# Optimization experiments

Hardware: AMD Instinct MI355X
Metric: run time of the kernel (lower is better)

Reference implementation:

```python
import jax, jax.numpy as jnp
import numpy as np

B, S, L, F = 32, 512, 13, 768
H = 512


def setup_inputs() -> dict:
    key = jax.random.key(0)
    ks = jax.random.split(key, 9)
    x = jax.random.normal(ks[0], (B, S, L, F), dtype=jnp.float32)
    lengths = jax.random.randint(ks[1], (B,), 0, S)
    lw = jnp.ones((L,), dtype=jnp.float32)  # WeightedAverage weights
    s1 = 1.0 / np.sqrt(2 * F)
    s2 = 1.0 / np.sqrt(H)
    s3 = 1.0 / np.sqrt(H // 2)
    W1 = jax.random.uniform(ks[2], (2 * F, H), jnp.float32, -s1, s1)
    b1 = jax.random.uniform(ks[3], (H,), jnp.float32, -s1, s1)
    W2 = jax.random.uniform(ks[4], (H, H // 2), jnp.float32, -s2, s2)
    b2 = jax.random.uniform(ks[5], (H // 2,), jnp.float32, -s2, s2)
    W3 = jax.random.uniform(ks[6], (H // 2, 1), jnp.float32, -s3, s3)
    b3 = jax.random.uniform(ks[7], (1,), jnp.float32, -s3, s3)
    return {"x": x, "lengths": lengths, "lw": lw, "W1": W1, "b1": b1,
            "W2": W2, "b2": b2, "W3": W3, "b3": b3}


def reference(x, lengths, lw, W1, b1, W2, b2, W3, b3):
    # layer-weighted average: softmax over L, contract layer dim
    w = jax.nn.softmax(lw)
    word = jnp.einsum("bslf,l->bsf", x, w)  # [B,S,F]

    # masked mean/std over the first lengths[i] positions of each sequence
    seq_len = word.shape[1]
    mask = (jnp.arange(seq_len)[None, :] < lengths[:, None]).astype(word.dtype)  # [B,S]
    n = jnp.sum(mask, axis=1, keepdims=True)  # [B,1]
    mean = jnp.sum(word * mask[:, :, None], axis=1) / jnp.maximum(n, 1.0)  # [B,F]
    diff = (word - mean[:, None, :]) * mask[:, :, None]
    # torch.std is unbiased (ddof=1); std defined 0 when n<=1
    var = jnp.sum(diff * diff, axis=1) / jnp.maximum(n - 1.0, 1.0)
    std = jnp.where(n > 1.0, jnp.sqrt(var), 0.0)
    feats = jnp.concatenate([mean, std], axis=-1)  # [B,2F]

    # MLP (dropout is inference no-op)
    h = jax.nn.relu(feats @ W1 + b1)
    h = jax.nn.relu(h @ W2 + b2)
    return h @ W3 + b3  # [B,1]
```

## Files before the change

kernel.cpp:

```cpp
#include <hip/hip_runtime.h>
#include <hip/hip_bf16.h>

#define LNUM 13
#define FDIM 768
#define SDIM 512
#define BNUM 32
#define H1DIM 512
#define H2DIM 256
#define GA0 992
#define GPAD (GA0 + BNUM)


__global__ __launch_bounds__(192) void kA_partials(
    const float* __restrict__ x, const int* __restrict__ lengths,
    const float* __restrict__ lw, float* __restrict__ partial) {
  __shared__ int lenS[BNUM];
  __shared__ int BB[BNUM + 1];
  __shared__ float wS[LNUM];
  const int tid = threadIdx.x;

  if (tid < BNUM) lenS[tid] = lengths[tid];
  __syncthreads();
  if (tid == 0) {
    int T = 0;
    #pragma unroll
    for (int b = 0; b < BNUM; ++b) T += lenS[b];
    int acc = 0; BB[0] = 0;
    #pragma unroll
    for (int b = 0; b < BNUM; ++b) {
      int nb = (T > 0 && lenS[b] > 0) ? (lenS[b] * GA0 + T - 1) / T : 0;
      acc += nb; BB[b + 1] = acc;
    }
    float m = lw[0];
    #pragma unroll
    for (int l = 1; l < LNUM; ++l) m = fmaxf(m, lw[l]);
    float e[LNUM]; float s = 0.f;
    #pragma unroll
    for (int l = 0; l < LNUM; ++l) { e[l] = expf(lw[l] - m); s += e[l]; }
    #pragma unroll
    for (int l = 0; l < LNUM; ++l) wS[l] = e[l] / s;
  }
  __syncthreads();

  const int g = blockIdx.x;
  if (g >= BB[BNUM]) return;

  int lo = 0, hi = BNUM;
  while (hi - lo > 1) { int mid = (lo + hi) >> 1; if (g >= BB[mid]) lo = mid; else hi = mid; }
  const int b   = lo;
  const int i   = g - BB[b];
  const int n   = BB[b + 1] - BB[b];
  const int len = lenS[b];
  const int base = len / n, rem = len % n;
  const int s0 = i * base + min(i, rem);
  const int cnt = base + (i < rem ? 1 : 0);

  float4 sum = make_float4(0.f, 0.f, 0.f, 0.f);
  float4 sq  = make_float4(0.f, 0.f, 0.f, 0.f);
  const float* xb = x + (size_t)b * SDIM * (LNUM * FDIM) + (size_t)tid * 4;

  for (int s = s0; s < s0 + cnt; ++s) {
    const float* xs = xb + (size_t)s * (LNUM * FDIM);
    float4 word = make_float4(0.f, 0.f, 0.f, 0.f);
    #pragma unroll
    for (int l = 0; l < LNUM; ++l) {
      float4 v = *reinterpret_cast<const float4*>(xs + l * FDIM);
      const float wl = wS[l];
      word.x = fmaf(wl, v.x, word.x);
      word.y = fmaf(wl, v.y, word.y);
      word.z = fmaf(wl, v.z, word.z);
      word.w = fmaf(wl, v.w, word.w);
    }
    sum.x += word.x; sum.y += word.y; sum.z += word.z; sum.w += word.w;
    sq.x = fmaf(word.x, word.x, sq.x);
    sq.y = fmaf(word.y, word.y, sq.y);
    sq.z = fmaf(word.z, word.z, sq.z);
    sq.w = fmaf(word.w, word.w, sq.w);
  }

  float* p = partial + (size_t)g * (2 * FDIM) + (size_t)tid * 4;
  *reinterpret_cast<float4*>(p) = sum;
  *reinterpret_cast<float4*>(p + FDIM) = sq;
}

__global__ __launch_bounds__(256) void kStats(
    const float* __restrict__ partial, const int* __restrict__ lengths,
    float* __restrict__ feats) {
  const int b  = blockIdx.x / 12;
  const int cg = blockIdx.x % 12;
  const int cl = threadIdx.x & 63;
  const int k  = threadIdx.x >> 6;
  const int f  = cg * 64 + cl;

  __shared__ int lenS[BNUM];
  __shared__ int BB[BNUM + 1];
  if (threadIdx.x < BNUM) lenS[threadIdx.x] = lengths[threadIdx.x];
  __syncthreads();
  if (threadIdx.x == 0) {
    int T = 0;
    #pragma unroll
    for (int bb = 0; bb < BNUM; ++bb) T += lenS[bb];
    int acc = 0; BB[0] = 0;
    #pragma unroll
    for (int bb = 0; bb < BNUM; ++bb) {
      int nb = (T > 0 && lenS[bb] > 0) ? (lenS[bb] * GA0 + T - 1) / T : 0;
      acc += nb; BB[bb + 1] = acc;
    }
  }
  __syncthreads();

  const int cBeg = BB[b], cEnd = BB[b + 1];
  float ms = 0.f, mq = 0.f;
  for (int cc = cBeg + k; cc < cEnd; cc += 4) {
    const float* p = partial + (size_t)cc * (2 * FDIM);
    ms += p[f];
    mq += p[FDIM + f];
  }
  __shared__ float rs[4][64], rq[4][64];
  rs[k][cl] = ms; rq[k][cl] = mq;
  __syncthreads();

  if (threadIdx.x < 64) {
    ms = rs[0][cl] + rs[1][cl] + rs[2][cl] + rs[3][cl];
    mq = rq[0][cl] + rq[1][cl] + rq[2][cl] + rq[3][cl];
    const int n = lenS[b];
    const float fn = (float)n;
    const float mean = ms / fmaxf(fn, 1.f);
    const float var = (mq - fn * mean * mean) / fmaxf(fn - 1.f, 1.f);
    const float sd = (n > 1) ? sqrtf(fmaxf(var, 0.f)) : 0.f;
    feats[(size_t)b * 2 * FDIM + f] = mean;
    feats[(size_t)b * 2 * FDIM + FDIM + f] = sd;
  }
}

__global__ __launch_bounds__(512) void kFC1(
    const float* __restrict__ feats, const float* __restrict__ W1,
    const float* __restrict__ b1, float* __restrict__ h1) {
  const int b  = blockIdx.x >> 2;
  const int jt = blockIdx.x & 3;
  const int t  = threadIdx.x;
  const int jl = t & 127;
  const int kh = t >> 7;
  const int j  = jt * 128 + jl;

  __shared__ float fs[2 * FDIM];
  __shared__ float red[4][128];

  for (int i = t; i < 2 * FDIM; i += 512)
    fs[i] = feats[(size_t)b * 2 * FDIM + i];
  __syncthreads();

  const float* wcol = W1 + (size_t)kh * 384 * H1DIM + j;
  const float* fk = fs + kh * 384;
  float acc = 0.f;
  #pragma unroll 16
  for (int i = 0; i < 384; ++i)
    acc = fmaf(fk[i], wcol[(size_t)i * H1DIM], acc);
  red[kh][jl] = acc;
  __syncthreads();

  if (t < 128) {
    float a = red[0][t] + red[1][t] + red[2][t] + red[3][t] + b1[jt * 128 + t];
    h1[(size_t)b * H1DIM + jt * 128 + t] = fmaxf(a, 0.f);
  }
}

__global__ __launch_bounds__(512) void kFC23(
    const float* __restrict__ h1, const float* __restrict__ W2,
    const float* __restrict__ b2, const float* __restrict__ W3,
    const float* __restrict__ b3, float* __restrict__ out) {
  const int b = blockIdx.x;
  const int t = threadIdx.x;
  const int jl = t & 255;
  const int kh = t >> 8;

  __shared__ float hs[H1DIM];
  __shared__ float red[2 * H2DIM];
  __shared__ float wred[8];

  if (t < H1DIM) hs[t] = h1[(size_t)b * H1DIM + t];
  __syncthreads();

  const float* wcol = W2 + (size_t)kh * 256 * H2DIM + jl;
  const float* hk = hs + kh * 256;
  float acc = 0.f;
  #pragma unroll 16
  for (int i = 0; i < 256; ++i)
    acc = fmaf(hk[i], wcol[(size_t)i * H2DIM], acc);
  red[kh * H2DIM + jl] = acc;
  __syncthreads();

  float v = 0.f;
  if (t < H2DIM) {
    const float h2 = fmaxf(red[t] + red[H2DIM + t] + b2[t], 0.f);
    v = h2 * W3[t];
  }
  #pragma unroll
  for (int off = 32; off > 0; off >>= 1) v += __shfl_down(v, off, 64);
  if ((t & 63) == 0) wred[t >> 6] = v;
  __syncthreads();
  if (t == 0) {
    float r = b3[0];
    #pragma unroll
    for (int i = 0; i < 8; ++i) r += wred[i];
    out[b] = r;
  }
}

extern "C" void kernel_launch(void* const* d_in, const int* in_sizes, int n_in,
                              void* d_out, int out_size, void* d_ws, size_t ws_size,
                              hipStream_t stream) {
  const float* x       = (const float*)d_in[0];
  const int*   lengths = (const int*)  d_in[1];
  const float* lw      = (const float*)d_in[2];
  const float* W1      = (const float*)d_in[3];
  const float* b1      = (const float*)d_in[4];
  const float* W2      = (const float*)d_in[5];
  const float* b2      = (const float*)d_in[6];
  const float* W3      = (const float*)d_in[7];
  const float* b3      = (const float*)d_in[8];
  float* out = (float*)d_out;

  float* partial = (float*)d_ws;
  float* feats   = partial + (size_t)GPAD * 2 * FDIM;
  float* h1      = feats + (size_t)BNUM * 2 * FDIM;

  kA_partials<<<dim3(GPAD), dim3(192), 0, stream>>>(x, lengths, lw, partial);
  kStats<<<dim3(BNUM * 12), dim3(256), 0, stream>>>(partial, lengths, feats);
  kFC1<<<dim3(BNUM * 4), dim3(512), 0, stream>>>(feats, W1, b1, h1);
  kFC23<<<dim3(BNUM), dim3(512), 0, stream>>>(h1, W2, b2, W3, b3, out);
}
```

Before: 89.27 us.

## Fuse FC1 and FC2/FC3 into one MLP kernel and raise partial-block count

Merges the two MLP kernels into a single per-batch kernel. FC1 now uses float4 weight loads per thread across all 512 outputs, and h1 stays in shared memory, which removes one launch and a global round trip. Separately, the number of sequence-chunk blocks in the partials kernel goes from 992 to 1504 to improve occupancy on the bandwidth-bound reduction. The fused MLP runs only 32 blocks, so FC1 parallelism drops from 128 blocks to 32.

```diff
diff --git a/kernel.cpp b/kernel.cpp
--- a/kernel.cpp
+++ b/kernel.cpp
@@ -7,7 +7,7 @@
 #define BNUM 32
 #define H1DIM 512
 #define H2DIM 256
-#define GA0 992
+#define GA0 1504
 #define GPAD (GA0 + BNUM)
 
 
@@ -133,61 +133,61 @@
   }
 }
 
-__global__ __launch_bounds__(512) void kFC1(
-    const float* __restrict__ feats, const float* __restrict__ W1,
-    const float* __restrict__ b1, float* __restrict__ h1) {
-  const int b  = blockIdx.x >> 2;
-  const int jt = blockIdx.x & 3;
-  const int t  = threadIdx.x;
-  const int jl = t & 127;
-  const int kh = t >> 7;
-  const int j  = jt * 128 + jl;
+__global__ __launch_bounds__(512) void kMLP(
+    const float* __restrict__ feats,
+    const float* __restrict__ W1, const float* __restrict__ b1,
+    const float* __restrict__ W2, const float* __restrict__ b2,
+    const float* __restrict__ W3, const float* __restrict__ b3,
+    float* __restrict__ out) {
+  const int b = blockIdx.x;
+  const int t = threadIdx.x;
 
   __shared__ float fs[2 * FDIM];
-  __shared__ float red[4][128];
+  __shared__ float r1[4][H1DIM];
+  __shared__ float h1s[H1DIM];
+  __shared__ float red[2 * H2DIM];
+  __shared__ float wred[8];
 
   for (int i = t; i < 2 * FDIM; i += 512)
     fs[i] = feats[(size_t)b * 2 * FDIM + i];
   __syncthreads();
 
-  const float* wcol = W1 + (size_t)kh * 384 * H1DIM + j;
-  const float* fk = fs + kh * 384;
-  float acc = 0.f;
-  #pragma unroll 16
-  for (int i = 0; i < 384; ++i)
-    acc = fmaf(fk[i], wcol[(size_t)i * H1DIM], acc);
-  red[kh][jl] = acc;
-  __syncthreads();
-
-  if (t < 128) {
-    float a = red[0][t] + red[1][t] + red[2][t] + red[3][t] + b1[jt * 128 + t];
-    h1[(size_t)b * H1DIM + jt * 128 + t] = fmaxf(a, 0.f);
-  }
-}
-
-__global__ __launch_bounds__(512) void kFC23(
-    const float* __restrict__ h1, const float* __restrict__ W2,
-    const float* __restrict__ b2, const float* __restrict__ W3,
-    const float* __restrict__ b3, float* __restrict__ out) {
-  const int b = blockIdx.x;
-  const int t = threadIdx.x;
-  const int jl = t & 255;
-  const int kh = t >> 8;
-
-  __shared__ float hs[H1DIM];
-  __shared__ float red[2 * H2DIM];
-  __shared__ float wred[8];
-
-  if (t < H1DIM) hs[t] = h1[(size_t)b * H1DIM + t];
-  __syncthreads();
-
-  const float* wcol = W2 + (size_t)kh * 256 * H2DIM + jl;
-  const float* hk = hs + kh * 256;
-  float acc = 0.f;
-  #pragma unroll 16
-  for (int i = 0; i < 256; ++i)
-    acc = fmaf(hk[i], wcol[(size_t)i * H2DIM], acc);
-  red[kh * H2DIM + jl] = acc;
+  {
+    const int jq = t & 127;
+    const int kh = t >> 7;
+    const float* fk = fs + kh * 384;
+    const float* wrow = W1 + (size_t)kh * 384 * H1DIM + 4 * jq;
+    float4 acc = make_float4(0.f, 0.f, 0.f, 0.f);
+    #pragma unroll 8
+    for (int i = 0; i < 384; ++i) {
+      float4 wv = *reinterpret_cast<const float4*>(wrow + (size_t)i * H1DIM);
+      const float f = fk[i];
+      acc.x = fmaf(f, wv.x, acc.x);
+      acc.y = fmaf(f, wv.y, acc.y);
+      acc.z = fmaf(f, wv.z, acc.z);
+      acc.w = fmaf(f, wv.w, acc.w);
+    }
+    r1[kh][4 * jq]     = acc.x;
+    r1[kh][4 * jq + 1] = acc.y;
+    r1[kh][4 * jq + 2] = acc.z;
+    r1[kh][4 * jq + 3] = acc.w;
+  }
+  __syncthreads();
+  if (t < H1DIM)
+    h1s[t] = fmaxf(r1[0][t] + r1[1][t] + r1[2][t] + r1[3][t] + b1[t], 0.f);
+  __syncthreads();
+
+  {
+    const int jl = t & 255;
+    const int kh = t >> 8;
+    const float* wcol = W2 + (size_t)kh * 256 * H2DIM + jl;
+    const float* hk = h1s + kh * 256;
+    float acc = 0.f;
+    #pragma unroll 16
+    for (int i = 0; i < 256; ++i)
+      acc = fmaf(hk[i], wcol[(size_t)i * H2DIM], acc);
+    red[kh * H2DIM + jl] = acc;
+  }
   __syncthreads();
 
   float v = 0.f;
@@ -223,10 +223,8 @@
 
   float* partial = (float*)d_ws;
   float* feats   = partial + (size_t)GPAD * 2 * FDIM;
-  float* h1      = feats + (size_t)BNUM * 2 * FDIM;
 
   kA_partials<<<dim3(GPAD), dim3(192), 0, stream>>>(x, lengths, lw, partial);
   kStats<<<dim3(BNUM * 12), dim3(256), 0, stream>>>(partial, lengths, feats);
-  kFC1<<<dim3(BNUM * 4), dim3(512), 0, stream>>>(feats, W1, b1, h1);
-  kFC23<<<dim3(BNUM), dim3(512), 0, stream>>>(h1, W2, b2, W3, b3, out);
-}
+  kMLP<<<dim3(BNUM), dim3(512), 0, stream>>>(feats, W1, b1, W2, b2, W3, b3, out);
+}
```

Result: slower. 112.7 us (+26.2%).

## Fuse partial-sum and stats kernels with a device-wide atomic counter barrier

Applied to the files above, without the earlier changes.

Merges the x-reduction kernel and the per-feature statistics kernel into one launch. Every block bumps an atomic counter after writing its partials, and the first 384 blocks spin until all blocks are done before reducing partials into mean and std. The goal is to drop one kernel launch boundary. In exchange it adds a memset launch and spin-wait latency, and it depends on all blocks being co-resident or scheduled before the waiters starve them.

```diff
diff --git a/kernel.cpp b/kernel.cpp
--- a/kernel.cpp
+++ b/kernel.cpp
@@ -9,15 +9,18 @@
 #define H2DIM 256
 #define GA0 992
 #define GPAD (GA0 + BNUM)
-
-
-__global__ __launch_bounds__(192) void kA_partials(
+#define NSTATS (BNUM * 12)
+
+__global__ __launch_bounds__(192) void kAS(
     const float* __restrict__ x, const int* __restrict__ lengths,
-    const float* __restrict__ lw, float* __restrict__ partial) {
+    const float* __restrict__ lw, float* __restrict__ partial,
+    float* __restrict__ feats, unsigned int* __restrict__ done) {
   __shared__ int lenS[BNUM];
   __shared__ int BB[BNUM + 1];
   __shared__ float wS[LNUM];
+  __shared__ float rs[3][64], rq[3][64];
   const int tid = threadIdx.x;
+  const int g = blockIdx.x;
 
   if (tid < BNUM) lenS[tid] = lengths[tid];
   __syncthreads();
@@ -42,87 +45,77 @@
   }
   __syncthreads();
 
-  const int g = blockIdx.x;
-  if (g >= BB[BNUM]) return;
-
-  int lo = 0, hi = BNUM;
-  while (hi - lo > 1) { int mid = (lo + hi) >> 1; if (g >= BB[mid]) lo = mid; else hi = mid; }
-  const int b   = lo;
-  const int i   = g - BB[b];
-  const int n   = BB[b + 1] - BB[b];
-  const int len = lenS[b];
-  const int base = len / n, rem = len % n;
-  const int s0 = i * base + min(i, rem);
-  const int cnt = base + (i < rem ? 1 : 0);
-
-  float4 sum = make_float4(0.f, 0.f, 0.f, 0.f);
-  float4 sq  = make_float4(0.f, 0.f, 0.f, 0.f);
-  const float* xb = x + (size_t)b * SDIM * (LNUM * FDIM) + (size_t)tid * 4;
-
-  for (int s = s0; s < s0 + cnt; ++s) {
-    const float* xs = xb + (size_t)s * (LNUM * FDIM);
-    float4 word = make_float4(0.f, 0.f, 0.f, 0.f);
-    #pragma unroll
-    for (int l = 0; l < LNUM; ++l) {
-      float4 v = *reinterpret_cast<const float4*>(xs + l * FDIM);
-      const float wl = wS[l];
-      word.x = fmaf(wl, v.x, word.x);
-      word.y = fmaf(wl, v.y, word.y);
-      word.z = fmaf(wl, v.z, word.z);
-      word.w = fmaf(wl, v.w, word.w);
+  if (g < BB[BNUM]) {
+    int lo = 0, hi = BNUM;
+    while (hi - lo > 1) { int mid = (lo + hi) >> 1; if (g >= BB[mid]) lo = mid; else hi = mid; }
+    const int b   = lo;
+    const int i   = g - BB[b];
+    const int n   = BB[b + 1] - BB[b];
+    const int len = lenS[b];
+    const int base = len / n, rem = len % n;
+    const int s0 = i * base + min(i, rem);
+    const int cnt = base + (i < rem ? 1 : 0);
+
+    float4 sum = make_float4(0.f, 0.f, 0.f, 0.f);
+    float4 sq  = make_float4(0.f, 0.f, 0.f, 0.f);
+    const float* xb = x + (size_t)b * SDIM * (LNUM * FDIM) + (size_t)tid * 4;
+
+    for (int s = s0; s < s0 + cnt; ++s) {
+      const float* xs = xb + (size_t)s * (LNUM * FDIM);
+      float4 word = make_float4(0.f, 0.f, 0.f, 0.f);
+      #pragma unroll
+      for (int l = 0; l < LNUM; ++l) {
+        float4 v = *reinterpret_cast<const float4*>(xs + l * FDIM);
+        const float wl = wS[l];
+        word.x = fmaf(wl, v.x, word.x);
+        word.y = fmaf(wl, v.y, word.y);
+        word.z = fmaf(wl, v.z, word.z);
+        word.w = fmaf(wl, v.w, word.w);
+      }
+      sum.x += word.x; sum.y += word.y; sum.z += word.z; sum.w += word.w;
+      sq.x = fmaf(word.x, word.x, sq.x);
+      sq.y = fmaf(word.y, word.y, sq.y);
+      sq.z = fmaf(word.z, word.z, sq.z);
+      sq.w = fmaf(word.w, word.w, sq.w);
     }
-    sum.x += word.x; sum.y += word.y; sum.z += word.z; sum.w += word.w;
-    sq.x = fmaf(word.x, word.x, sq.x);
-    sq.y = fmaf(word.y, word.y, sq.y);
-    sq.z = fmaf(word.z, word.z, sq.z);
-    sq.w = fmaf(word.w, word.w, sq.w);
-  }
-
-  float* p = partial + (size_t)g * (2 * FDIM) + (size_t)tid * 4;
-  *reinterpret_cast<float4*>(p) = sum;
-  *reinterpret_cast<float4*>(p + FDIM) = sq;
-}
-
-__global__ __launch_bounds__(256) void kStats(
-    const float* __restrict__ partial, const int* __restrict__ lengths,
-    float* __restrict__ feats) {
-  const int b  = blockIdx.x / 12;
-  const int cg = blockIdx.x % 12;
-  const int cl = threadIdx.x & 63;
-  const int k  = threadIdx.x >> 6;
+
+    float* p = partial + (size_t)g * (2 * FDIM) + (size_t)tid * 4;
+    *reinterpret_cast<float4*>(p) = sum;
+    *reinterpret_cast<float4*>(p + FDIM) = sq;
+  }
+
+  __threadfence();
+  __syncthreads();
+  if (tid == 0)
+    __hip_atomic_fetch_add(done, 1u, __ATOMIC_RELEASE, __HIP_MEMORY_SCOPE_AGENT);
+  if (g >= NSTATS) return;
+
+  if (tid == 0) {
+    while (__hip_atomic_load(done, __ATOMIC_ACQUIRE, __HIP_MEMORY_SCOPE_AGENT) < GPAD)
+      __builtin_amdgcn_s_sleep(8);
+  }
+  __syncthreads();
+  __threadfence();
+
+  const int b  = g / 12;
+  const int cg = g % 12;
+  const int cl = tid & 63;
+  const int k  = tid >> 6;
   const int f  = cg * 64 + cl;
-
-  __shared__ int lenS[BNUM];
-  __shared__ int BB[BNUM + 1];
-  if (threadIdx.x < BNUM) lenS[threadIdx.x] = lengths[threadIdx.x];
-  __syncthreads();
-  if (threadIdx.x == 0) {
-    int T = 0;
-    #pragma unroll
-    for (int bb = 0; bb < BNUM; ++bb) T += lenS[bb];
-    int acc = 0; BB[0] = 0;
-    #pragma unroll
-    for (int bb = 0; bb < BNUM; ++bb) {
-      int nb = (T > 0 && lenS[bb] > 0) ? (lenS[bb] * GA0 + T - 1) / T : 0;
-      acc += nb; BB[bb + 1] = acc;
-    }
-  }
-  __syncthreads();
 
   const int cBeg = BB[b], cEnd = BB[b + 1];
   float ms = 0.f, mq = 0.f;
-  for (int cc = cBeg + k; cc < cEnd; cc += 4) {
+  for (int cc = cBeg + k; cc < cEnd; cc += 3) {
     const float* p = partial + (size_t)cc * (2 * FDIM);
-    ms += p[f];
-    mq += p[FDIM + f];
-  }
-  __shared__ float rs[4][64], rq[4][64];
+    ms += __hip_atomic_load(&p[f],        __ATOMIC_RELAXED, __HIP_MEMORY_SCOPE_AGENT);
+    mq += __hip_atomic_load(&p[FDIM + f], __ATOMIC_RELAXED, __HIP_MEMORY_SCOPE_AGENT);
+  }
   rs[k][cl] = ms; rq[k][cl] = mq;
   __syncthreads();
 
-  if (threadIdx.x < 64) {
-    ms = rs[0][cl] + rs[1][cl] + rs[2][cl] + rs[3][cl];
-    mq = rq[0][cl] + rq[1][cl] + rq[2][cl] + rq[3][cl];
+  if (tid < 64) {
+    ms = rs[0][cl] + rs[1][cl] + rs[2][cl];
+    mq = rq[0][cl] + rq[1][cl] + rq[2][cl];
     const int n = lenS[b];
     const float fn = (float)n;
     const float mean = ms / fmaxf(fn, 1.f);
@@ -224,9 +217,10 @@
   float* partial = (float*)d_ws;
   float* feats   = partial + (size_t)GPAD * 2 * FDIM;
   float* h1      = feats + (size_t)BNUM * 2 * FDIM;
-
-  kA_partials<<<dim3(GPAD), dim3(192), 0, stream>>>(x, lengths, lw, partial);
-  kStats<<<dim3(BNUM * 12), dim3(256), 0, stream>>>(partial, lengths, feats);
+  unsigned int* done = (unsigned int*)(h1 + (size_t)BNUM * H1DIM);
+
+  hipMemsetAsync(done, 0, sizeof(unsigned int), stream);
+  kAS<<<dim3(GPAD), dim3(192), 0, stream>>>(x, lengths, lw, partial, feats, done);
   kFC1<<<dim3(BNUM * 4), dim3(512), 0, stream>>>(feats, W1, b1, h1);
   kFC23<<<dim3(BNUM), dim3(512), 0, stream>>>(h1, W2, b2, W3, b3, out);
 }
```

Measured after the change: 317.1 us. +255.2%, slower.
